# Kernel optimization log

Hardware: AMD Instinct MI355X
Metric: run time of the kernel (lower is better)

Reference implementation:

```python
import jax, jax.numpy as jnp
import numpy as np
from jax import lax

B, T_ENC, T_DEC, H, L, F, NC, S = 1024, 128, 64, 128, 2, 16, 4, 8
X_DIM = 2
IN_DIM = X_DIM + F          # encoder GRU input_size = 18
H_ENC = 2 * H               # encoder hidden = 256 (mean/logvar)
H_DEC = H + NC              # decoder hidden = 132 (concat_cond_ts=False)


def _gru_params(key, in_dim, hid):
    k1, k2, k3, k4 = jax.random.split(key, 4)
    s = 1.0 / np.sqrt(hid)
    u = lambda k, shp: jax.random.uniform(k, shp, minval=-s, maxval=s, dtype=jnp.float32)
    return u(k1, (3 * hid, in_dim)), u(k2, (3 * hid, hid)), u(k3, (3 * hid,)), u(k4, (3 * hid,))


def gru_cell(x, h, Wih, Whh, bih, bhh):
    # torch GRU cell: r,z,n gate ordering
    gi = x @ Wih.T + bih
    gh = h @ Whh.T + bhh
    hd = h.shape[-1]
    ir, iz, inn = gi[:, :hd], gi[:, hd:2 * hd], gi[:, 2 * hd:]
    hr, hz, hn = gh[:, :hd], gh[:, hd:2 * hd], gh[:, 2 * hd:]
    r = jax.nn.sigmoid(ir + hr)
    zg = jax.nn.sigmoid(iz + hz)
    n = jnp.tanh(inn + r * hn)
    return (1.0 - zg) * n + zg * h


def setup_inputs() -> dict:
    key = jax.random.key(0)
    ks = jax.random.split(key, 12)
    x = jax.random.normal(ks[0], (B, T_ENC, X_DIM), dtype=jnp.float32)
    features = jax.random.normal(ks[1], (B, T_ENC + T_DEC, F), dtype=jnp.float32)
    lengths = jax.random.randint(ks[2], (B,), T_ENC // 2, T_ENC + 1)
    mask = (jnp.arange(T_ENC)[None, :] < lengths[:, None]).astype(jnp.int32)
    eps = jax.random.normal(ks[3], (S, L, B, H), dtype=jnp.float32)
    enc0 = _gru_params(ks[4], IN_DIM, H_ENC)
    enc1 = _gru_params(ks[5], H_ENC, H_ENC)
    dec0 = _gru_params(ks[6], 2, H_DEC)
    dec1 = _gru_params(ks[7], H_DEC, H_DEC)
    sm = 1.0 / np.sqrt(H)
    W1 = jax.random.uniform(ks[8], (H // 2, H), minval=-sm, maxval=sm, dtype=jnp.float32)
    b1 = jax.random.uniform(ks[9], (H // 2,), minval=-sm, maxval=sm, dtype=jnp.float32)
    s2 = 1.0 / np.sqrt(H // 2)
    W2 = jax.random.uniform(ks[10], (2, H // 2), minval=-s2, maxval=s2, dtype=jnp.float32)
    b2 = jax.random.uniform(ks[11], (2,), minval=-s2, maxval=s2, dtype=jnp.float32)
    return dict(
        x=x, features=features, mask=mask, eps=eps,
        nsteps_encode=T_ENC, nsteps_decode=T_DEC, n_elbo_samp=S,
        enc_Wih0=enc0[0], enc_Whh0=enc0[1], enc_bih0=enc0[2], enc_bhh0=enc0[3],
        enc_Wih1=enc1[0], enc_Whh1=enc1[1], enc_bih1=enc1[2], enc_bhh1=enc1[3],
        dec_Wih0=dec0[0], dec_Whh0=dec0[1], dec_bih0=dec0[2], dec_bhh0=dec0[3],
        dec_Wih1=dec1[0], dec_Whh1=dec1[1], dec_bih1=dec1[2], dec_bhh1=dec1[3],
        W1=W1, b1=b1, W2=W2, b2=b2,
    )


def reference(x, features, mask, eps, nsteps_encode, nsteps_decode, n_elbo_samp,
              enc_Wih0, enc_Whh0, enc_bih0, enc_bhh0,
              enc_Wih1, enc_Whh1, enc_bih1, enc_bhh1,
              dec_Wih0, dec_Whh0, dec_bih0, dec_bhh0,
              dec_Wih1, dec_Whh1, dec_bih1, dec_bhh1,
              W1, b1, W2, b2):
    n_hidden = W1.shape[1]
    batch = x.shape[0]
    enc_input = jnp.concatenate([x, features[:, :nsteps_encode, :]], axis=-1)
    m = mask.astype(bool)

    def mlp(h):
        return jax.nn.softplus(jax.nn.relu(h @ W1.T + b1) @ W2.T + b2)

    # --- encoder: 2-layer GRU with pack_padded semantics (freeze h / zero out past length) ---
    def enc_step(h, xm):
        xt, mt = xm
        h0n = gru_cell(xt, h[0], enc_Wih0, enc_Whh0, enc_bih0, enc_bhh0)
        h0n = jnp.where(mt[:, None], h0n, h[0])
        h1n = gru_cell(h0n, h[1], enc_Wih1, enc_Whh1, enc_bih1, enc_bhh1)
        h1n = jnp.where(mt[:, None], h1n, h[1])
        out = jnp.where(mt[:, None], h1n, 0.0)
        return jnp.stack([h0n, h1n]), out

    h_init = jnp.zeros((2, batch, enc_Whh0.shape[1]), dtype=x.dtype)
    hT, outs = lax.scan(enc_step, h_init, (enc_input.transpose(1, 0, 2), m.T))
    enc_out = outs.transpose(1, 0, 2)                 # [B, T_enc, 2H]
    enc_pred = mlp(enc_out[..., :n_hidden])           # [B, T_enc, 2]
    z_mean = hT[:, :, :n_hidden]                      # [L, B, H]
    z_logvar = hT[:, :, n_hidden:]

    last = enc_pred[:, -1, :]                         # [B, 2]
    feat_cond = features[:, nsteps_encode, :4]        # cond_inds = [0,1,2,3]

    # --- decoder: sequential single-step GRU, h0 = cat(z, cond feats) ---
    def decode_one(e):
        z = e * jnp.exp(0.5 * z_logvar) + z_mean      # [L, B, H]
        fc = jnp.broadcast_to(feat_cond[None], (z.shape[0],) + feat_cond.shape)
        h0 = jnp.concatenate([z, fc], axis=-1)        # [L, B, H+NC]
        def step(carry, _):
            inp, h = carry
            d0 = gru_cell(inp, h[0], dec_Wih0, dec_Whh0, dec_bih0, dec_bhh0)
            d1 = gru_cell(d0, h[1], dec_Wih1, dec_Whh1, dec_bih1, dec_bhh1)
            out = mlp(d1[:, :n_hidden])
            return (out, jnp.stack([d0, d1])), out
        _, outs_d = lax.scan(step, (last, h0), None, length=nsteps_decode - 1)
        return jnp.concatenate([last[None], outs_d], axis=0)   # [T_dec, B, 2]

    dec = jax.vmap(decode_one)(eps)                   # [S, T_dec, B, 2]
    dec_preds = dec.transpose(0, 2, 1, 3)             # [S, B, T_dec, 2]
    enc_stack = jnp.broadcast_to(enc_pred[None, :, :-1, :],
                                 (n_elbo_samp, batch, enc_pred.shape[1] - 1, 2))
    return enc_stack, dec_preds
```

## Files before the change

### kernel.cpp

```cpp
#include <hip/hip_runtime.h>
#include <hip/hip_bf16.h>
#include <math.h>

typedef __hip_bfloat16 bf16;
typedef short v8s __attribute__((ext_vector_type(8)));
typedef float v4f __attribute__((ext_vector_type(4)));

#define NB   1024
#define NT   128
#define NH   128
#define HE   256
#define HD   132
#define HDP  160
#define HDS  164
#define GDP  144
#define NS   8
#define KX   32
#define RG   16
#define NRG  64

namespace wsoff {
constexpr size_t al(size_t x){ return (x + 255) & ~size_t(255); }
constexpr size_t FLAG  = 0;
constexpr size_t CNT   = 256;
// ... 86 lines not shown

__global__ void k_detect(char* ws, const void* eps){
  const unsigned short* p = (const unsigned short*)eps;
  int lane = threadIdx.x;
  unsigned short u = p[2*lane];
  int e = (u>>7)&0xFF;
  bool pl = (e>=118 && e<=130);
  unsigned long long m = __ballot(pl);
  if (lane==0) *(int*)(ws+wsoff::FLAG) = (__popcll(m) >= 32) ? 1 : 0;
}

__global__ void k_stage_xs(char* ws, const void* x, const void* feat){
  int isbf = *(const int*)(ws+wsoff::FLAG);
  size_t i = (size_t)blockIdx.x*blockDim.x + threadIdx.x;
  if (i >= (size_t)NT*NB*KX) return;
  int c = i % KX; size_t q = i / KX; int b = q % NB; int t = q / NB;
  float v = 0.f;
  if (c < 2)        v = ld_any(x,    ((size_t)b*NT + t)*2 + c, isbf);
  else if (c < 18)  v = ld_any(feat, ((size_t)b*192 + t)*16 + (c-2), isbf);
  ((bf16*)(ws+wsoff::XS))[i] = __float2bfloat16(v);
}
__global__ void k_stage_maskT(char* ws, const int* mask){
  size_t i = (size_t)blockIdx.x*blockDim.x + threadIdx.x;
  if (i >= (size_t)NT*NB) return;
  int b = i % NB, t = i / NB;
  ((int*)(ws+wsoff::MASKT))[i] = mask[(size_t)b*NT + t];
}
__global__ void k_stage_pad(char* ws, const void* src, size_t dstoff, int R, int SC, int DC){
  int isbf = *(const int*)(ws+wsoff::FLAG);
  size_t i = (size_t)blockIdx.x*blockDim.x + threadIdx.x;
  if (i >= (size_t)R*DC) return;
  int r = i / DC, c = i % DC;
  float v = (c < SC) ? ld_any(src, (size_t)r*SC + c, isbf) : 0.f;
  ((bf16*)(ws+dstoff))[i] = __float2bfloat16(v);
}
__global__ void k_stage_dec(char* ws, const void* src, size_t dstoff){
  int isbf = *(const int*)(ws+wsoff::FLAG);
  size_t i = (size_t)blockIdx.x*blockDim.x + threadIdx.x;
  if (i >= (size_t)432*HDP) return;
  int R = i / HDP, c = i % HDP;
  int g = R / GDP, ii = R % GDP;
  float v = (ii < HD && c < HD) ? ld_any(src, ((size_t)(g*HD+ii))*HD + c, isbf) : 0.f;
  ((bf16*)(ws+dstoff))[i] = __float2bfloat16(v);
}
struct SmallSegs { const void* src[12]; int dstoff[12]; int n[12]; };
__global__ void k_stage_small(char* ws, SmallSegs segs){
  int isbf = *(const int*)(ws+wsoff::FLAG);
  int s = blockIdx.x;
  float* dst = (float*)(ws + (size_t)segs.dstoff[s]);
  for (int i = threadIdx.x; i < segs.n[s]; i += blockDim.x)
    dst[i] = ld_any(segs.src[s], i, isbf);
}

#define ENC_LDS 156928
__global__ __attribute__((amdgpu_flat_work_group_size(512,512), amdgpu_waves_per_eu(1)))
void k_encoder(char* ws){
  extern __shared__ __align__(16) char smem[];
  const int bid = blockIdx.x, tid = threadIdx.x;
  const int lane = tid & 63, w = tid >> 6, lr = lane & 15, q = lane >> 4;
  const int* maskT = (const int*)(ws + wsoff::MASKT);

  if (bid < NRG){
    constexpr int NL0 = 18;
    constexpr int NR0 = 54 - NL0;
    const int rb = bid, rowbase = rb*RG;
    short* wlds = (short*)smem;
    short* abuf = (short*)(smem + 8*NL0*1024);
    int* cL0 = cntp(ws, rb);
    int* cXa = cntp(ws, NRG + rb*2);
    int* cXb = cntp(ws, NRG + rb*2 + 1);
    const short* WH = (const short*)(ws + wsoff::WHH0);
    const short* WI = (const short*)(ws + wsoff::WIH0);
    for (int idx = tid; idx < 8*NL0*512; idx += 512){
      int slot = idx >> 9, le = idx & 511, ln = le >> 3, j = le & 7, lrr = ln & 15, qq = ln >> 4;
      int w2 = slot / NL0, i = slot % NL0;
      int kb = i % 9, t2 = i / 9, g = t2 % 3, cs = t2 / 3;
      int row = g*HE + w2*32 + cs*16 + lrr;
      wlds[idx] = (kb < 8) ? WH[(size_t)row*256 + kb*32 + qq*8 + j]
                           : WI[(size_t)row*32  + qq*8 + j];
    }
    for (int idx = tid; idx < RG*296; idx += 512) abuf[idx] = 0;
    v8s wreg[NR0];
    #pragma unroll
    for (int i = NL0; i < 54; ++i){
      int kb = i % 9, t2 = i / 9, g = t2 % 3, cs = t2 / 3;
      int row = g*HE + w*32 + cs*16 + lr;
      wreg[i-NL0] = (kb < 8) ? fragld(bfp(ws,wsoff::WHH0), (size_t)row*256 + kb*32 + q*8)
                             : fragld(bfp(ws,wsoff::WIH0), (size_t)row*32 + q*8);
    }
    const float* bih = f32p(ws,wsoff::BIH0);
    const float* bhh = f32p(ws,wsoff::BHH0);
    float birv[2], bizv[2], binv[2], bhnv[2];
    #pragma unroll
    for (int cs=0;cs<2;cs++){
      int d = w*32 + cs*16 + lr;
      birv[cs]=bih[d]+bhh[d]; bizv[cs]=bih[HE+d]+bhh[HE+d];
      binv[cs]=bih[2*HE+d];   bhnv[cs]=bhh[2*HE+d];
    }
    float h0a[2][4] = {};
    float* hTf = f32p(ws, wsoff::H0F0);
    bf16* ring0 = bfp(ws, wsoff::RING0) + (size_t)rb*4*RG*256;
    const bf16* Xs = bfp(ws,wsoff::XS);
    __syncthreads();
    for (int t = 0; t < 128; ++t){
      if (tid < 64){
        int row = tid >> 2, ck = tid & 3;
// ... 59 lines not shown
    short* abuf = (short*)(smem + 8*NL1*1024);
    short* w1s  = (short*)(smem + 8*NL1*1024 + RG*520*2);
    int* cL0 = cntp(ws, rb);
    int* cXo = cntp(ws, NRG + rb*2 + ch);
    int* cXp = cntp(ws, NRG + rb*2 + (ch^1));
    const short* WX = (const short*)(ws + wsoff::WIH1);
    const short* WHs= (const short*)(ws + wsoff::WHH1);
    for (int idx = tid; idx < 8*NL1*512; idx += 512){
      int slot = idx >> 9, le = idx & 511, ln = le >> 3, j = le & 7, lrr = ln & 15, qq = ln >> 4;
      int w2 = slot / NL1, i = slot % NL1;
      int kb = i & 15, g = i >> 4;
      int row = g*HE + ch*128 + w2*16 + lrr;
      wlds[idx] = (kb < 8) ? WX [(size_t)row*256 + kb*32 + qq*8 + j]
                           : WHs[(size_t)row*256 + (kb-8)*32 + qq*8 + j];
    }
    if (ch == 0){
      const short* W1s = (const short*)(ws + wsoff::W1B);
      for (int idx = tid; idx < 16*512; idx += 512){
        int u = idx >> 9, le = idx & 511, ln = le >> 3, j = le & 7, lrr = ln & 15, qq = ln >> 4;
        int c = u >> 2, kb = u & 3;
        w1s[idx] = W1s[(size_t)(c*16 + lrr)*NH + kb*32 + qq*8 + j];
      }
    }
    for (int idx = tid; idx < RG*520; idx += 512) abuf[idx] = 0;
    v8s wreg[NR1];
    #pragma unroll
    for (int i = NL1; i < 48; ++i){
      int kb = i & 15, g = i >> 4;
      int row = g*HE + ch*128 + w*16 + lr;
      wreg[i-NL1] = (kb < 8) ? fragld(bfp(ws,wsoff::WIH1), (size_t)row*256 + kb*32 + q*8)
                             : fragld(bfp(ws,wsoff::WHH1), (size_t)row*256 + (kb-8)*32 + q*8);
    }
    const float* bih = f32p(ws,wsoff::BIH1);
    const float* bhh = f32p(ws,wsoff::BHH1);
    const int d = ch*128 + w*16 + lr;
    const float birv=bih[d]+bhh[d], bizv=bih[HE+d]+bhh[HE+d];
    const float binv=bih[2*HE+d],   bhnv=bhh[2*HE+d];
    float h1a[4] = {};
    float b1v[4], w20[4], w21[4];
    #pragma unroll
    for (int c=0;c<4;c++){
      int col=c*16+lr;
      b1v[c]=f32p(ws,wsoff::B1F)[col];
      w20[c]=f32p(ws,wsoff::W2F)[col]; w21[c]=f32p(ws,wsoff::W2F)[64+col];
    }
    const float b20 = f32p(ws,wsoff::B2F)[0], b21 = f32p(ws,wsoff::B2F)[1];
    float* hTf = f32p(ws, wsoff::H1F0);
    const bf16* ring0 = bfp(ws, wsoff::RING0) + (size_t)rb*4*RG*256;
    bf16* ring1o       = bfp(ws, wsoff::RING1) + (size_t)(rb*2+ch)*2*RG*128;
    const bf16* ring1p = bfp(ws, wsoff::RING1) + (size_t)(rb*2+(ch^1))*2*RG*128;
    float* encp = f32p(ws,wsoff::ENCP);
    __syncthreads();
    for (int s = 0; s < 128; ++s){
      {
        pollge(cL0, s+1);
        const bf16* hs = ring0 + (size_t)(s&3)*RG*256;
        int row = tid >> 5, ck = tid & 31;
        v8s v = ldg_coh16(hs + (size_t)row*256 + ck*8);
        *(v8s*)(abuf + row*520 + ck*8) = v;
      }
      if (s >= 1 && tid < 256){
        pollge(cXp, s);
        const bf16* hp = ring1p + (size_t)((s-1)&1)*RG*128;
        int row = tid >> 4, ck = tid & 15;
        v8s v = ldg_coh16(hp + (size_t)row*128 + ck*8);
        *(v8s*)(abuf + row*520 + 256 + (ch^1)*128 + ck*8) = v;
      }
      __syncthreads();
      v4f accr=(v4f){0,0,0,0}, accz=(v4f){0,0,0,0};
      v4f accxn=(v4f){0,0,0,0}, acchn=(v4f){0,0,0,0};
      #pragma unroll
      for (int kb=0;kb<16;kb++){
        v8s af = lds_frag8(abuf + lr*520 + kb*32 + q*8);
        #pragma unroll
        for (int g=0;g<3;g++){
          int i = g*16 + kb;
          v8s b = (i < NL1) ? ldsfrag(wlds, w*NL1 + i, lane) : wreg[i-NL1];
          v4f* A = (g==0)?&accr:(g==1)?&accz:((kb<8)?&accxn:&acchn);
          *A = mfma16(af, b, *A);
        }
      }
      int mk[4];
      #pragma unroll
      for (int rr=0;rr<4;rr++) mk[rr] = maskT[(size_t)s*NB + rowbase + q*4 + rr];
      __syncthreads();
      bf16* slot = ring1o + (size_t)(s&1)*RG*128;
      #pragma unroll
      for (int rr=0;rr<4;rr++){
        int row = q*4 + rr;
        float rg = sigm(accr[rr] + birv);
        float zg = sigm(accz[rr] + bizv);
        float nn = tanh_f(accxn[rr] + binv + rg*(acchn[rr]+bhnv));
        float hv = (1.f-zg)*nn + zg*h1a[rr];
        float h2 = mk[rr] ? hv : h1a[rr];
        h1a[rr] = h2;
        int ch_col = w*16 + lr;
        abuf[row*520 + 256 + ch*128 + ch_col] = bf16bits(h2);
        stg_coh_pair(slot + ((size_t)row*128 + (ch_col & ~1)), lr, h2);
        if (s == 127) hTf[(size_t)(rowbase+row)*HE + d] = h2;
      }
      __syncthreads();
      if (tid == 0) cntset(cXo, s+1);
      if (ch == 0 && w == 0){
        int vl = maskT[(size_t)s*NB + rowbase + lr];
        v4f acc[4];
        #pragma unroll
        for (int c=0;c<4;c++) acc[c]=(v4f){0,0,0,0};
        #pragma unroll
        for (int kb=0;kb<4;kb++){
          v8s af = vl ? lds_frag8(abuf + lr*520 + 256 + kb*32 + q*8)
                      : (v8s){0,0,0,0,0,0,0,0};
          #pragma unroll
          for (int c=0;c<4;c++) acc[c] = mfma16(af, ldsfrag(w1s, c*4+kb, lane), acc[c]);
        }
        float* outp = encp + (size_t)s*NB*2;
        #pragma unroll
        for (int rr=0;rr<4;rr++){
          float p0=0.f, p1=0.f;
          #pragma unroll
          for (int c=0;c<4;c++){
            float hv = acc[c][rr] + b1v[c]; hv = hv>0.f ? hv : 0.f;
            p0 += hv*w20[c]; p1 += hv*w21[c];
          }
          #pragma unroll
          for (int m=1;m<16;m<<=1){ p0 += __shfl_xor(p0,m,64); p1 += __shfl_xor(p1,m,64); }
          if (lr == 0){
            int grow = rowbase + q*4 + rr;
            outp[(size_t)grow*2]   = softplusf(p0+b20);
            outp[(size_t)grow*2+1] = softplusf(p1+b21);
          }
        }
      }
    }
  }
}

__global__ __attribute__((amdgpu_flat_work_group_size(512,512), amdgpu_waves_per_eu(1)))
void k_decoder(char* ws, const void* eps, const void* feat, void* out){
  extern __shared__ __align__(16) char dsm[];
  short* s_h0b = (short*)dsm;
  short* s_h1b = s_h0b + 32*HDS;
  float* s_inp = (float*)(dsm + 20992);
  float* s_red = (float*)(dsm + 21248);
  short* s_wh  = (short*)(dsm + 21760);
  short* s_cw0 = (short*)(dsm + 144640);
  short* s_cwx = (short*)(dsm + 147808);
  short* s_cwh = (short*)(dsm + 150976);
  float* s_tail= (float*)(dsm + 154144);
  float* s_th  = (float*)(dsm + 156192);
  float* s_tt0 = (float*)(dsm + 157216);
  float* s_tt1 = (float*)(dsm + 157376);

  const int isbf = *(const int*)(ws+wsoff::FLAG);
  const int tid = threadIdx.x;
  const int lane = tid & 63, w = tid >> 6, lr = lane & 15, q = lane >> 4;
  const int rowbase = blockIdx.x*32;
  constexpr size_t N0v = (size_t)NS*NB*127*2;

  const bf16* W0g  = bfp(ws,wsoff::WDHH0);
  const bf16* WX1g = bfp(ws,wsoff::WDIH1);

  for (int i = tid; i < 2*32*HDS; i += 512) s_h0b[i] = 0;
  {
    const short* src = (const short*)(ws + wsoff::WDHH1);
    for (int idx = tid; idx < 120*512; idx += 512){
      int u = idx >> 9, le = idx & 511, ln = le >> 3, e = le & 7, lrr = ln & 15, qq = ln >> 4;
      int kb = u % 5, t2 = u / 5, cc = t2 & 7, g = t2 >> 3;
      s_wh[idx] = src[(size_t)(g*GDP + cc*16 + lrr)*HDP + kb*32 + qq*8 + e];
    }
    const short* g0 = (const short*)(ws + wsoff::WDHH0);
    const short* gx = (const short*)(ws + wsoff::WDIH1);
    const short* gh = (const short*)(ws + wsoff::WDHH1);
    for (int i = tid; i < 3*4*132; i += 512){
      int k = i % 132, t2 = i / 132, c4 = t2 & 3, g = t2 >> 2;
      size_t so = (size_t)(g*GDP + 128 + c4)*HDP + k;
      s_cw0[i] = g0[so]; s_cwx[i] = gx[so]; s_cwh[i] = gh[so];
    }
  }
  if (tid < 4){
    const float* wih = f32p(ws,wsoff::WDIH0F);
    const float* bi0 = f32p(ws,wsoff::BDIH0); const float* bh0 = f32p(ws,wsoff::BDHH0);
    const float* bi1 = f32p(ws,wsoff::BDIH1); const float* bh1 = f32p(ws,wsoff::BDHH1);
    int dd = 128 + tid;
    float* T = s_tt0 + tid*10;
    T[0]=wih[(0*HD+dd)*2]; T[1]=wih[(0*HD+dd)*2+1];
    T[2]=wih[(1*HD+dd)*2]; T[3]=wih[(1*HD+dd)*2+1];
    T[4]=wih[(2*HD+dd)*2]; T[5]=wih[(2*HD+dd)*2+1];
    T[6]=bi0[dd]+bh0[dd]; T[7]=bi0[HD+dd]+bh0[HD+dd]; T[8]=bi0[2*HD+dd]; T[9]=bh0[2*HD+dd];
    float* T1 = s_tt1 + tid*4;
    T1[0]=bi1[dd]+bh1[dd]; T1[1]=bi1[HD+dd]+bh1[HD+dd]; T1[2]=bi1[2*HD+dd]; T1[3]=bh1[2*HD+dd];
  }
  if (tid < 64){
    int r0 = tid >> 1, c = tid & 1;
    int b = (rowbase + r0) & 1023;
    float v = f32p(ws,wsoff::ENCP)[((size_t)127*NB + b)*2 + c];
    s_inp[tid] = v;
    st_out(out, N0v + ((size_t)(rowbase+r0)*64)*2 + c, v, isbf);
  }
  __syncthreads();

  const int d = w*16 + lr;
  float e0a[10], e1a[4];
  {
    const float* wih = f32p(ws,wsoff::WDIH0F);
    const float* bi0 = f32p(ws,wsoff::BDIH0); const float* bh0 = f32p(ws,wsoff::BDHH0);
    const float* bi1 = f32p(ws,wsoff::BDIH1); const float* bh1 = f32p(ws,wsoff::BDHH1);
    e0a[0]=wih[(0*HD+d)*2]; e0a[1]=wih[(0*HD+d)*2+1];
    e0a[2]=wih[(1*HD+d)*2]; e0a[3]=wih[(1*HD+d)*2+1];
    e0a[4]=wih[(2*HD+d)*2]; e0a[5]=wih[(2*HD+d)*2+1];
    e0a[6]=bi0[d]+bh0[d]; e0a[7]=bi0[HD+d]+bh0[HD+d]; e0a[8]=bi0[2*HD+d]; e0a[9]=bh0[2*HD+d];
    e1a[0]=bi1[d]+bh1[d]; e1a[1]=bi1[HD+d]+bh1[HD+d]; e1a[2]=bi1[2*HD+d]; e1a[3]=bh1[2*HD+d];
  }
  float h0a[2][4], h1a[2][4];
  {
    const float* h0T = f32p(ws,wsoff::H0F0);
    const float* h1T = f32p(ws,wsoff::H1F0);
    #pragma unroll
    for (int m=0;m<2;m++)
      #pragma unroll
      for (int r=0;r<4;r++){
        int row = m*16 + q*4 + r, grow = rowbase + row;
        int s = grow >> 10, b = grow & 1023;
        float e0 = ld_any(eps, ((size_t)(s*2+0)*NB + b)*NH + d, isbf);
        float e1 = ld_any(eps, ((size_t)(s*2+1)*NB + b)*NH + d, isbf);
        float v0 = e0*__expf(0.5f*h0T[(size_t)b*HE + NH + d]) + h0T[(size_t)b*HE + d];
        float v1 = e1*__expf(0.5f*h1T[(size_t)b*HE + NH + d]) + h1T[(size_t)b*HE + d];
        h0a[m][r] = v0; h1a[m][r] = v1;
        s_h0b[row*HDS + d] = bf16bits(v0);
        s_h1b[row*HDS + d] = bf16bits(v1);
      }
  }
  if (tid < 128){
    int c4 = tid >> 5, row = tid & 31;
    int b = (rowbase + row) & 1023;
    float fc = ld_any(feat, (size_t)b*3072 + 2048 + c4, isbf);
    s_th[row*4 + c4] = fc;
    s_th[128 + row*4 + c4] = fc;
    s_h0b[row*HDS + 128 + c4] = bf16bits(fc);
    s_h1b[row*HDS + 128 + c4] = bf16bits(fc);
  }
  v8s w0f[3][5], wxf[3][5];
  #pragma unroll
  for (int g=0;g<3;g++)
    #pragma unroll
    for (int kb=0;kb<5;kb++){
      size_t off = (size_t)(g*GDP + w*16 + lr)*HDP + kb*32 + q*8;
      w0f[g][kb] = fragld(W0g, off);
      wxf[g][kb] = fragld(WX1g, off);
    }
  v8s w1f[2][4]; float b1v[2], w20v[2], w21v[2];
  if (w == 5 || w == 6){
    const int tb = (w-5)*2;
    const bf16* W1g = bfp(ws,wsoff::W1B);
    #pragma unroll
    for (int ct=0;ct<2;ct++){
      #pragma unroll
      for (int kb=0;kb<4;kb++)
        w1f[ct][kb] = fragld(W1g, (size_t)((tb+ct)*16+lr)*NH + kb*32 + q*8);
      b1v[ct]  = f32p(ws,wsoff::B1F)[(tb+ct)*16+lr];
      w20v[ct] = f32p(ws,wsoff::W2F)[(tb+ct)*16+lr];
      w21v[ct] = f32p(ws,wsoff::W2F)[64+(tb+ct)*16+lr];
    }
  }
  const float b20 = f32p(ws,wsoff::B2F)[0], b21 = f32p(ws,wsoff::B2F)[1];
  __syncthreads();

  const int ttg = tid >> 7, ttc4 = (tid >> 5) & 3, ttrow = tid & 31;
  for (int k = 0; k < 63; ++k){
    v4f p1[3][2];
    #pragma unroll
    for (int g=0;g<3;g++){ p1[g][0]=(v4f){0,0,0,0}; p1[g][1]=(v4f){0,0,0,0}; }
    #pragma unroll
    for (int m=0;m<2;m++)
      #pragma unroll
      for (int kb=0;kb<5;kb++){
        v8s A = lds_frag8(s_h0b + (m*16+lr)*HDS + kb*32 + q*8);
        #pragma unroll
        for (int g=0;g<3;g++) p1[g][m] = mfma16(A, w0f[g][kb], p1[g][m]);
      }
    if (k >= 1 && tid < 64){
      int row = tid >> 1, c = tid & 1;
      float p = s_red[row*2 + c] + s_red[64 + row*2 + c];
      float v = softplusf(p + (c ? b21 : b20));
      s_inp[tid] = v;
      st_out(out, N0v + ((size_t)(rowbase+row)*64 + k)*2 + c, v, isbf);
    }
    if (tid < 384){
      const unsigned* st = (const unsigned*)s_h0b + ttrow*(HDS/2);
      const unsigned* wp = (const unsigned*)s_cw0 + (ttg*4+ttc4)*66;
      float t0=0.f, t1=0.f, t2v=0.f, t3v=0.f;
      #pragma unroll 2
      for (int k2 = 0; k2 < 64; k2 += 4){
        unsigned sa=st[k2],   wa=wp[k2];
        unsigned sb=st[k2+1], wb=wp[k2+1];
        unsigned sc=st[k2+2], wc=wp[k2+2];
        unsigned sd=st[k2+3], wd=wp[k2+3];
        t0  += uasf(sa<<16)*uasf(wa<<16) + uasf(sa & 0xffff0000u)*uasf(wa & 0xffff0000u);
        t1  += uasf(sb<<16)*uasf(wb<<16) + uasf(sb & 0xffff0000u)*uasf(wb & 0xffff0000u);
        t2v += uasf(sc<<16)*uasf(wc<<16) + uasf(sc & 0xffff0000u)*uasf(wc & 0xffff0000u);
        t3v += uasf(sd<<16)*uasf(wd<<16) + uasf(sd & 0xffff0000u)*uasf(wd & 0xffff0000u);
      }
      { unsigned sa=st[64], wa=wp[64], sb=st[65], wb=wp[65];
        t0 += uasf(sa<<16)*uasf(wa<<16) + uasf(sa & 0xffff0000u)*uasf(wa & 0xffff0000u);
        t1 += uasf(sb<<16)*uasf(wb<<16) + uasf(sb & 0xffff0000u)*uasf(wb & 0xffff0000u); }
      s_tail[(ttg*4+ttc4)*32 + ttrow] = (t0+t1)+(t2v+t3v);
    }
    __syncthreads();
    #pragma unroll
    for (int m=0;m<2;m++)
      #pragma unroll
      for (int r=0;r<4;r++){
        int row = m*16 + q*4 + r;
        float i0 = s_inp[row*2], i1 = s_inp[row*2+1];
        float rr = sigm(i0*e0a[0]+i1*e0a[1] + p1[0][m][r] + e0a[6]);
        float zz = sigm(i0*e0a[2]+i1*e0a[3] + p1[1][m][r] + e0a[7]);
        float nn = tanh_f(i0*e0a[4]+i1*e0a[5] + e0a[8] + rr*(p1[2][m][r] + e0a[9]));
        float h = (1.f-zz)*nn + zz*h0a[m][r];
        h0a[m][r] = h;
        s_h0b[row*HDS + d] = bf16bits(h);
      }
    if (tid < 128){
      int c4 = tid >> 5, row = tid & 31;
      float ar = s_tail[(0*4+c4)*32+row], az = s_tail[(1*4+c4)*32+row], an = s_tail[(2*4+c4)*32+row];
      const float* T = s_tt0 + c4*10;
      float i0 = s_inp[row*2], i1 = s_inp[row*2+1];
      float rr = sigm(i0*T[0]+i1*T[1] + ar + T[6]);
      float zz = sigm(i0*T[2]+i1*T[3] + az + T[7]);
      float nn = tanh_f(i0*T[4]+i1*T[5] + T[8] + rr*(an + T[9]));
      float ho = s_th[row*4 + c4];
      float h = (1.f-zz)*nn + zz*ho;
      s_th[row*4 + c4] = h;
      s_h0b[row*HDS + 128 + c4] = bf16bits(h);
    }
    __syncthreads();
    v4f p2[4][2];
    #pragma unroll
    for (int g=0;g<4;g++){ p2[g][0]=(v4f){0,0,0,0}; p2[g][1]=(v4f){0,0,0,0}; }
    #pragma unroll
    for (int m=0;m<2;m++)
      #pragma unroll
      for (int kb=0;kb<5;kb++){
        v8s ax = lds_frag8(s_h0b + (m*16+lr)*HDS + kb*32 + q*8);
        v8s ah = lds_frag8(s_h1b + (m*16+lr)*HDS + kb*32 + q*8);
        #pragma unroll
        for (int g=0;g<3;g++){
          int aix = (g==2) ? 2 : g, aih = (g==2) ? 3 : g;
          p2[aix][m] = mfma16(ax, wxf[g][kb], p2[aix][m]);
          p2[aih][m] = mfma16(ah, ldsfrag(s_wh, (g*8+w)*5 + kb, lane), p2[aih][m]);
        }
      }
    {
      const unsigned* h0p = (const unsigned*)s_h0b + ttrow*(HDS/2);
      const unsigned* h1p = (const unsigned*)s_h1b + ttrow*(HDS/2);
      float td = 0.f;
      if (ttg <= 1){
        const unsigned* wx = (const unsigned*)s_cwx + (ttg*4+ttc4)*66;
        const unsigned* wh = (const unsigned*)s_cwh + (ttg*4+ttc4)*66;
        float x0=0.f, x1=0.f, y0=0.f, y1=0.f;
        #pragma unroll 2
        for (int k2 = 0; k2 < 66; k2 += 2){
          unsigned sa=h0p[k2],   wa=wx[k2];
          unsigned sb=h0p[k2+1], wb=wx[k2+1];
          unsigned ha=h1p[k2],   va=wh[k2];
          unsigned hb=h1p[k2+1], vb=wh[k2+1];
          x0 += uasf(sa<<16)*uasf(wa<<16) + uasf(sa & 0xffff0000u)*uasf(wa & 0xffff0000u);
          x1 += uasf(sb<<16)*uasf(wb<<16) + uasf(sb & 0xffff0000u)*uasf(wb & 0xffff0000u);
          y0 += uasf(ha<<16)*uasf(va<<16) + uasf(ha & 0xffff0000u)*uasf(va & 0xffff0000u);
          y1 += uasf(hb<<16)*uasf(vb<<16) + uasf(hb & 0xffff0000u)*uasf(vb & 0xffff0000u);
        }
        td = (x0+x1)+(y0+y1);
      } else if (ttg == 2){
        const unsigned* wx = (const unsigned*)s_cwx + (2*4+ttc4)*66;
        float x0=0.f, x1=0.f;
        #pragma unroll 2
        for (int k2 = 0; k2 < 66; k2 += 2){
          unsigned sa=h0p[k2], wa=wx[k2], sb=h0p[k2+1], wb=wx[k2+1];
          x0 += uasf(sa<<16)*uasf(wa<<16) + uasf(sa & 0xffff0000u)*uasf(wa & 0xffff0000u);
          x1 += uasf(sb<<16)*uasf(wb<<16) + uasf(sb & 0xffff0000u)*uasf(wb & 0xffff0000u);
        }
        td = x0+x1;
      } else {
        const unsigned* wh = (const unsigned*)s_cwh + (2*4+ttc4)*66;
        float y0=0.f, y1=0.f;
        #pragma unroll 2
        for (int k2 = 0; k2 < 66; k2 += 2){
          unsigned sa=h1p[k2], wa=wh[k2], sb=h1p[k2+1], wb=wh[k2+1];
          y0 += uasf(sa<<16)*uasf(wa<<16) + uasf(sa & 0xffff0000u)*uasf(wa & 0xffff0000u);
          y1 += uasf(sb<<16)*uasf(wb<<16) + uasf(sb & 0xffff0000u)*uasf(wb & 0xffff0000u);
        }
        td = y0+y1;
      }
      s_tail[(ttg*4+ttc4)*32 + ttrow] = td;
    }
    __syncthreads();
    #pragma unroll
    for (int m=0;m<2;m++)
      #pragma unroll
      for (int r=0;r<4;r++){
        int row = m*16 + q*4 + r;
        float rr = sigm(p2[0][m][r] + e1a[0]);
        float zz = sigm(p2[1][m][r] + e1a[1]);
        float nn = tanh_f(p2[2][m][r] + e1a[2] + rr*(p2[3][m][r] + e1a[3]));
        float h = (1.f-zz)*nn + zz*h1a[m][r];
        h1a[m][r] = h;
        s_h1b[row*HDS + d] = bf16bits(h);
      }
    if (tid < 128){
      int c4 = tid >> 5, row = tid & 31;
      float tr = s_tail[(0*4+c4)*32+row], tz = s_tail[(1*4+c4)*32+row];
      float txn = s_tail[(2*4+c4)*32+row], thn = s_tail[(3*4+c4)*32+row];
      const float* T1 = s_tt1 + c4*4;
      float rr = sigm(tr + T1[0]);
      float zz = sigm(tz + T1[1]);
      float nn = tanh_f(txn + T1[2] + rr*(thn + T1[3]));
      float ho = s_th[128 + row*4 + c4];
      float h = (1.f-zz)*nn + zz*ho;
      s_th[128 + row*4 + c4] = h;
      s_h1b[row*HDS + 128 + c4] = bf16bits(h);
    }
    __syncthreads();
    if (w == 5 || w == 6){
      v4f a3[2][2];
      #pragma unroll
      for (int ct=0;ct<2;ct++){ a3[ct][0]=(v4f){0,0,0,0}; a3[ct][1]=(v4f){0,0,0,0}; }
      #pragma unroll
      for (int m=0;m<2;m++)
        #pragma unroll
        for (int kb=0;kb<4;kb++){
          v8s A = lds_frag8(s_h1b + (m*16+lr)*HDS + kb*32 + q*8);
          #pragma unroll
          for (int ct=0;ct<2;ct++) a3[ct][m] = mfma16(A, w1f[ct][kb], a3[ct][m]);
        }
      #pragma unroll
      for (int m=0;m<2;m++)
        #pragma unroll
        for (int r=0;r<4;r++){
          float p0 = 0.f, p1v = 0.f;
          #pragma unroll
          for (int ct=0;ct<2;ct++){
            float hv = a3[ct][m][r] + b1v[ct]; hv = hv > 0.f ? hv : 0.f;
            p0 += hv*w20v[ct]; p1v += hv*w21v[ct];
          }
          #pragma unroll
          for (int mm=1;mm<16;mm<<=1){ p0 += __shfl_xor(p0,mm,64); p1v += __shfl_xor(p1v,mm,64); }
          if (lr == 0){
            int row = m*16 + q*4 + r;
            s_red[(w-5)*64 + row*2]   = p0;
            s_red[(w-5)*64 + row*2+1] = p1v;
          }
        }
    }
    __syncthreads();
  }
  if (tid < 64){
    int row = tid >> 1, c = tid & 1;
    float p = s_red[row*2 + c] + s_red[64 + row*2 + c];
    float v = softplusf(p + (c ? b21 : b20));
    st_out(out, N0v + ((size_t)(rowbase+row)*64 + 63)*2 + c, v, isbf);
  }
}

__global__ void k_assemble_enc(char* ws, void* out){
  int isbf = *(const int*)(ws+wsoff::FLAG);
  const float* encp = f32p(ws,wsoff::ENCP);
  constexpr size_t N0v = (size_t)NS*NB*127*2;
  for (size_t i = (size_t)blockIdx.x*blockDim.x + threadIdx.x; i < N0v;
       i += (size_t)gridDim.x*blockDim.x){
    int c = (int)(i & 1); size_t qq = i >> 1;
    int tt = (int)(qq % 127); size_t q2 = qq / 127; int b = (int)(q2 & 1023);
    st_out(out, i, encp[((size_t)tt*NB + b)*2 + c], isbf);
  }
}

extern "C" void kernel_launch(void* const* d_in, const int* in_sizes, int n_in,
                              void* d_out, int out_size, void* d_ws, size_t ws_size,
                              hipStream_t stream) {
  char* ws = (char*)d_ws;
  const int* mask = (const int*)d_in[2];
  auto gb = [](size_t n){ return dim3((unsigned)((n + 255)/256)); };

  hipMemsetAsync(ws+wsoff::CNT, 0, 192*64, stream);

  k_detect<<<1,64,0,stream>>>(ws, d_in[3]);

  k_stage_xs   <<<gb((size_t)NT*NB*KX),256,0,stream>>>(ws, d_in[0], d_in[1]);
  k_stage_maskT<<<gb((size_t)NT*NB),256,0,stream>>>(ws, mask);
  k_stage_pad<<<gb(768*32) ,256,0,stream>>>(ws, d_in[7],  wsoff::WIH0, 768, 18, 32);
  k_stage_pad<<<gb(768*256),256,0,stream>>>(ws, d_in[8],  wsoff::WHH0, 768, 256, 256);
  k_stage_pad<<<gb(768*256),256,0,stream>>>(ws, d_in[11], wsoff::WIH1, 768, 256, 256);
  k_stage_pad<<<gb(768*256),256,0,stream>>>(ws, d_in[12], wsoff::WHH1, 768, 256, 256);
  k_stage_pad<<<gb(64*128) ,256,0,stream>>>(ws, d_in[23], wsoff::W1B,  64, 128, 128);
  k_stage_dec<<<gb(432*HDP),256,0,stream>>>(ws, d_in[16], wsoff::WDHH0);
  k_stage_dec<<<gb(432*HDP),256,0,stream>>>(ws, d_in[19], wsoff::WDIH1);
  k_stage_dec<<<gb(432*HDP),256,0,stream>>>(ws, d_in[20], wsoff::WDHH1);

  SmallSegs ss;
  const void* srcs[12] = {d_in[9],d_in[10],d_in[13],d_in[14],d_in[15],
                          d_in[17],d_in[18],d_in[21],d_in[22],
                          d_in[24],d_in[25],d_in[26]};
  const size_t offs[12] = {wsoff::BIH0,wsoff::BHH0,wsoff::BIH1,wsoff::BHH1,wsoff::WDIH0F,
                           wsoff::BDIH0,wsoff::BDHH0,wsoff::BDIH1,wsoff::BDHH1,
                           wsoff::B1F,wsoff::W2F,wsoff::B2F};
  const int ns[12] = {768,768,768,768,792,396,396,396,396,64,128,2};
  for (int i=0;i<12;i++){ ss.src[i]=srcs[i]; ss.dstoff[i]=(int)offs[i]; ss.n[i]=ns[i]; }
  k_stage_small<<<12,256,0,stream>>>(ws, ss);

  hipFuncSetAttribute(reinterpret_cast<const void*>(k_encoder),
                      hipFuncAttributeMaxDynamicSharedMemorySize, ENC_LDS);
  hipFuncSetAttribute(reinterpret_cast<const void*>(k_decoder),
                      hipFuncAttributeMaxDynamicSharedMemorySize, 157440);

  k_encoder<<<192,512,ENC_LDS,stream>>>(ws);
  k_decoder<<<256,512,157440,stream>>>(ws, d_in[3], d_in[1], d_out);
  k_assemble_enc<<<2048,256,0,stream>>>(ws, d_out);
}
```

Baseline: 1.819 ms.

## Shrink decoder blocks to 16 rows, stream weights from global, overlap encoder layer-1 MFMAs

The decoder now handles 16 rows per block over 512 blocks instead of 32 rows over 256. It drops the large LDS copy of the layer-1 hidden weights and the register-resident weight fragments, reloading weight fragments from global/L2 on every step. This cuts LDS use from about 157KB to about 22KB and raises the waves_per_eu hint to 4, so several blocks can share a CU, at the price of repeated global weight loads. In the encoder's layer-1 path, the MFMAs for this chunk's own hidden half are issued before waiting on the partner chunk's data, to hide the cross-block poll latency.

After: 2.637 ms. 45.0% more time.

```diff
diff --git a/kernel.cpp b/kernel.cpp
--- a/kernel.cpp
+++ b/kernel.cpp
@@ -162,6 +162,14 @@
     dst[i] = ld_any(segs.src[s], i, isbf);
 }
 
+#define L1_STEP(kb) { \
+  v8s af = lds_frag8(abuf + lr*520 + (kb)*32 + q*8); \
+  { const int i = 0*16 + (kb); v8s b = (i < NL1) ? ldsfrag(wlds, w*NL1 + i, lane) : wreg[i-NL1]; accr = mfma16(af, b, accr); } \
+  { const int i = 1*16 + (kb); v8s b = (i < NL1) ? ldsfrag(wlds, w*NL1 + i, lane) : wreg[i-NL1]; accz = mfma16(af, b, accz); } \
+  { const int i = 2*16 + (kb); v8s b = (i < NL1) ? ldsfrag(wlds, w*NL1 + i, lane) : wreg[i-NL1]; \
+    if ((kb) < 8) accxn = mfma16(af, b, accxn); else acchn = mfma16(af, b, acchn); } \
+}
+
 #define ENC_LDS 156928
 __global__ __attribute__((amdgpu_flat_work_group_size(512,512), amdgpu_waves_per_eu(1)))
 void k_encoder(char* ws){
@@ -327,6 +335,8 @@
     float* encp = f32p(ws,wsoff::ENCP);
     __syncthreads();
     for (int s = 0; s < 128; ++s){
+      v4f accr=(v4f){0,0,0,0}, accz=(v4f){0,0,0,0};
+      v4f accxn=(v4f){0,0,0,0}, acchn=(v4f){0,0,0,0};
       {
         pollge(cL0, s+1);
         const bf16* hs = ring0 + (size_t)(s&3)*RG*256;
@@ -334,6 +344,8 @@
         v8s v = ldg_coh16(hs + (size_t)row*256 + ck*8);
         *(v8s*)(abuf + row*520 + ck*8) = v;
       }
+      if (ch == 0){ L1_STEP(8)  L1_STEP(9)  L1_STEP(10) L1_STEP(11) }
+      else        { L1_STEP(12) L1_STEP(13) L1_STEP(14) L1_STEP(15) }
       if (s >= 1 && tid < 256){
         pollge(cXp, s);
         const bf16* hp = ring1p + (size_t)((s-1)&1)*RG*128;
@@ -342,19 +354,10 @@
         *(v8s*)(abuf + row*520 + 256 + (ch^1)*128 + ck*8) = v;
       }
       __syncthreads();
-      v4f accr=(v4f){0,0,0,0}, accz=(v4f){0,0,0,0};
-      v4f accxn=(v4f){0,0,0,0}, acchn=(v4f){0,0,0,0};
-      #pragma unroll
-      for (int kb=0;kb<16;kb++){
-        v8s af = lds_frag8(abuf + lr*520 + kb*32 + q*8);
-        #pragma unroll
-        for (int g=0;g<3;g++){
-          int i = g*16 + kb;
-          v8s b = (i < NL1) ? ldsfrag(wlds, w*NL1 + i, lane) : wreg[i-NL1];
-          v4f* A = (g==0)?&accr:(g==1)?&accz:((kb<8)?&accxn:&acchn);
-          *A = mfma16(af, b, *A);
-        }
-      }
+      L1_STEP(0) L1_STEP(1) L1_STEP(2) L1_STEP(3)
+      L1_STEP(4) L1_STEP(5) L1_STEP(6) L1_STEP(7)
+      if (ch == 0){ L1_STEP(12) L1_STEP(13) L1_STEP(14) L1_STEP(15) }
+      else        { L1_STEP(8)  L1_STEP(9)  L1_STEP(10) L1_STEP(11) }
       int mk[4];
       #pragma unroll
       for (int rr=0;rr<4;rr++) mk[rr] = maskT[(size_t)s*NB + rowbase + q*4 + rr];
@@ -410,39 +413,35 @@
   }
 }
 
-__global__ __attribute__((amdgpu_flat_work_group_size(512,512), amdgpu_waves_per_eu(1)))
+#define DEC_LDS 22144
+__global__ __attribute__((amdgpu_flat_work_group_size(512,512), amdgpu_waves_per_eu(4)))
 void k_decoder(char* ws, const void* eps, const void* feat, void* out){
   extern __shared__ __align__(16) char dsm[];
   short* s_h0b = (short*)dsm;
-  short* s_h1b = s_h0b + 32*HDS;
-  float* s_inp = (float*)(dsm + 20992);
-  float* s_red = (float*)(dsm + 21248);
-  short* s_wh  = (short*)(dsm + 21760);
-  short* s_cw0 = (short*)(dsm + 144640);
-  short* s_cwx = (short*)(dsm + 147808);
-  short* s_cwh = (short*)(dsm + 150976);
-  float* s_tail= (float*)(dsm + 154144);
-  float* s_th  = (float*)(dsm + 156192);
-  float* s_tt0 = (float*)(dsm + 157216);
-  float* s_tt1 = (float*)(dsm + 157376);
+  short* s_h1b = s_h0b + 16*HDS;
+  float* s_inp = (float*)(dsm + 10496);
+  float* s_red = (float*)(dsm + 10624);
+  short* s_cw0 = (short*)(dsm + 10880);
+  short* s_cwx = (short*)(dsm + 14048);
+  short* s_cwh = (short*)(dsm + 17216);
+  float* s_tail= (float*)(dsm + 20384);
+  float* s_th  = (float*)(dsm + 21408);
+  float* s_tt0 = (float*)(dsm + 21920);
+  float* s_tt1 = (float*)(dsm + 22080);
 
   const int isbf = *(const int*)(ws+wsoff::FLAG);
   const int tid = threadIdx.x;
   const int lane = tid & 63, w = tid >> 6, lr = lane & 15, q = lane >> 4;
-  const int rowbase = blockIdx.x*32;
+  const int rowbase = blockIdx.x*16;
   constexpr size_t N0v = (size_t)NS*NB*127*2;
 
   const bf16* W0g  = bfp(ws,wsoff::WDHH0);
   const bf16* WX1g = bfp(ws,wsoff::WDIH1);
-
-  for (int i = tid; i < 2*32*HDS; i += 512) s_h0b[i] = 0;
+  const bf16* WH1g = bfp(ws,wsoff::WDHH1);
+  const size_t woff = (size_t)(w*16 + lr)*HDP + q*8;
+
+  for (int i = tid; i < 2*16*HDS; i += 512) s_h0b[i] = 0;
   {
-    const short* src = (const short*)(ws + wsoff::WDHH1);
-    for (int idx = tid; idx < 120*512; idx += 512){
-      int u = idx >> 9, le = idx & 511, ln = le >> 3, e = le & 7, lrr = ln & 15, qq = ln >> 4;
-      int kb = u % 5, t2 = u / 5, cc = t2 & 7, g = t2 >> 3;
-      s_wh[idx] = src[(size_t)(g*GDP + cc*16 + lrr)*HDP + kb*32 + qq*8 + e];
-    }
     const short* g0 = (const short*)(ws + wsoff::WDHH0);
     const short* gx = (const short*)(ws + wsoff::WDIH1);
     const short* gh = (const short*)(ws + wsoff::WDHH1);
@@ -465,7 +464,7 @@
     float* T1 = s_tt1 + tid*4;
     T1[0]=bi1[dd]+bh1[dd]; T1[1]=bi1[HD+dd]+bh1[HD+dd]; T1[2]=bi1[2*HD+dd]; T1[3]=bh1[2*HD+dd];
   }
-  if (tid < 64){
+  if (tid < 32){
     int r0 = tid >> 1, c = tid & 1;
     int b = (rowbase + r0) & 1023;
     float v = f32p(ws,wsoff::ENCP)[((size_t)127*NB + b)*2 + c];
@@ -486,83 +485,57 @@
     e0a[6]=bi0[d]+bh0[d]; e0a[7]=bi0[HD+d]+bh0[HD+d]; e0a[8]=bi0[2*HD+d]; e0a[9]=bh0[2*HD+d];
     e1a[0]=bi1[d]+bh1[d]; e1a[1]=bi1[HD+d]+bh1[HD+d]; e1a[2]=bi1[2*HD+d]; e1a[3]=bh1[2*HD+d];
   }
-  float h0a[2][4], h1a[2][4];
+  float h0a[4], h1a[4];
   {
     const float* h0T = f32p(ws,wsoff::H0F0);
     const float* h1T = f32p(ws,wsoff::H1F0);
     #pragma unroll
-    for (int m=0;m<2;m++)
-      #pragma unroll
-      for (int r=0;r<4;r++){
-        int row = m*16 + q*4 + r, grow = rowbase + row;
-        int s = grow >> 10, b = grow & 1023;
-        float e0 = ld_any(eps, ((size_t)(s*2+0)*NB + b)*NH + d, isbf);
-        float e1 = ld_any(eps, ((size_t)(s*2+1)*NB + b)*NH + d, isbf);
-        float v0 = e0*__expf(0.5f*h0T[(size_t)b*HE + NH + d]) + h0T[(size_t)b*HE + d];
-        float v1 = e1*__expf(0.5f*h1T[(size_t)b*HE + NH + d]) + h1T[(size_t)b*HE + d];
-        h0a[m][r] = v0; h1a[m][r] = v1;
-        s_h0b[row*HDS + d] = bf16bits(v0);
-        s_h1b[row*HDS + d] = bf16bits(v1);
-      }
-  }
-  if (tid < 128){
-    int c4 = tid >> 5, row = tid & 31;
+    for (int r=0;r<4;r++){
+      int row = q*4 + r, grow = rowbase + row;
+      int s = grow >> 10, b = grow & 1023;
+      float e0 = ld_any(eps, ((size_t)(s*2+0)*NB + b)*NH + d, isbf);
+      float e1 = ld_any(eps, ((size_t)(s*2+1)*NB + b)*NH + d, isbf);
+      float v0 = e0*__expf(0.5f*h0T[(size_t)b*HE + NH + d]) + h0T[(size_t)b*HE + d];
+      float v1 = e1*__expf(0.5f*h1T[(size_t)b*HE + NH + d]) + h1T[(size_t)b*HE + d];
+      h0a[r] = v0; h1a[r] = v1;
+      s_h0b[row*HDS + d] = bf16bits(v0);
+      s_h1b[row*HDS + d] = bf16bits(v1);
+    }
+  }
+  if (tid < 64){
+    int c4 = tid >> 4, row = tid & 15;
     int b = (rowbase + row) & 1023;
     float fc = ld_any(feat, (size_t)b*3072 + 2048 + c4, isbf);
     s_th[row*4 + c4] = fc;
-    s_th[128 + row*4 + c4] = fc;
+    s_th[64 + row*4 + c4] = fc;
     s_h0b[row*HDS + 128 + c4] = bf16bits(fc);
     s_h1b[row*HDS + 128 + c4] = bf16bits(fc);
   }
-  v8s w0f[3][5], wxf[3][5];
-  #pragma unroll
-  for (int g=0;g<3;g++)
-    #pragma unroll
-    for (int kb=0;kb<5;kb++){
-      size_t off = (size_t)(g*GDP + w*16 + lr)*HDP + kb*32 + q*8;
-      w0f[g][kb] = fragld(W0g, off);
-      wxf[g][kb] = fragld(WX1g, off);
-    }
-  v8s w1f[2][4]; float b1v[2], w20v[2], w21v[2];
-  if (w == 5 || w == 6){
-    const int tb = (w-5)*2;
-    const bf16* W1g = bfp(ws,wsoff::W1B);
-    #pragma unroll
-    for (int ct=0;ct<2;ct++){
-      #pragma unroll
-      for (int kb=0;kb<4;kb++)
-        w1f[ct][kb] = fragld(W1g, (size_t)((tb+ct)*16+lr)*NH + kb*32 + q*8);
-      b1v[ct]  = f32p(ws,wsoff::B1F)[(tb+ct)*16+lr];
-      w20v[ct] = f32p(ws,wsoff::W2F)[(tb+ct)*16+lr];
-      w21v[ct] = f32p(ws,wsoff::W2F)[64+(tb+ct)*16+lr];
-    }
-  }
   const float b20 = f32p(ws,wsoff::B2F)[0], b21 = f32p(ws,wsoff::B2F)[1];
   __syncthreads();
 
-  const int ttg = tid >> 7, ttc4 = (tid >> 5) & 3, ttrow = tid & 31;
+  const int t1g = tid >> 6, t1c4 = (tid >> 4) & 3, t1row = tid & 15;
+  const int t2g = tid >> 6, t2c4 = (tid >> 4) & 3, t2row = tid & 15;
   for (int k = 0; k < 63; ++k){
-    v4f p1[3][2];
-    #pragma unroll
-    for (int g=0;g<3;g++){ p1[g][0]=(v4f){0,0,0,0}; p1[g][1]=(v4f){0,0,0,0}; }
-    #pragma unroll
-    for (int m=0;m<2;m++)
-      #pragma unroll
-      for (int kb=0;kb<5;kb++){
-        v8s A = lds_frag8(s_h0b + (m*16+lr)*HDS + kb*32 + q*8);
-        #pragma unroll
-        for (int g=0;g<3;g++) p1[g][m] = mfma16(A, w0f[g][kb], p1[g][m]);
-      }
-    if (k >= 1 && tid < 64){
+    v4f p1[3];
+    p1[0]=(v4f){0,0,0,0}; p1[1]=(v4f){0,0,0,0}; p1[2]=(v4f){0,0,0,0};
+    #pragma unroll
+    for (int kb=0;kb<5;kb++){
+      v8s A = lds_frag8(s_h0b + lr*HDS + kb*32 + q*8);
+      #pragma unroll
+      for (int g=0;g<3;g++)
+        p1[g] = mfma16(A, fragld(W0g, (size_t)g*(GDP*HDP) + kb*32 + woff), p1[g]);
+    }
+    if (k >= 1 && tid < 32){
       int row = tid >> 1, c = tid & 1;
-      float p = s_red[row*2 + c] + s_red[64 + row*2 + c];
+      float p = s_red[row*2 + c] + s_red[32 + row*2 + c];
       float v = softplusf(p + (c ? b21 : b20));
       s_inp[tid] = v;
       st_out(out, N0v + ((size_t)(rowbase+row)*64 + k)*2 + c, v, isbf);
     }
-    if (tid < 384){
-      const unsigned* st = (const unsigned*)s_h0b + ttrow*(HDS/2);
-      const unsigned* wp = (const unsigned*)s_cw0 + (ttg*4+ttc4)*66;
+    if (tid < 192){
+      const unsigned* st = (const unsigned*)s_h0b + t1row*(HDS/2);
+      const unsigned* wp = (const unsigned*)s_cw0 + (t1g*4+t1c4)*66;
       float t0=0.f, t1=0.f, t2v=0.f, t3v=0.f;
       #pragma unroll 2
       for (int k2 = 0; k2 < 64; k2 += 4){
@@ -578,25 +551,23 @@
       { unsigned sa=st[64], wa=wp[64], sb=st[65], wb=wp[65];
         t0 += uasf(sa<<16)*uasf(wa<<16) + uasf(sa & 0xffff0000u)*uasf(wa & 0xffff0000u);
         t1 += uasf(sb<<16)*uasf(wb<<16) + uasf(sb & 0xffff0000u)*uasf(wb & 0xffff0000u); }
-      s_tail[(ttg*4+ttc4)*32 + ttrow] = (t0+t1)+(t2v+t3v);
+      s_tail[(t1g*4+t1c4)*16 + t1row] = (t0+t1)+(t2v+t3v);
     }
     __syncthreads();
     #pragma unroll
-    for (int m=0;m<2;m++)
-      #pragma unroll
-      for (int r=0;r<4;r++){
-        int row = m*16 + q*4 + r;
-        float i0 = s_inp[row*2], i1 = s_inp[row*2+1];
-        float rr = sigm(i0*e0a[0]+i1*e0a[1] + p1[0][m][r] + e0a[6]);
-        float zz = sigm(i0*e0a[2]+i1*e0a[3] + p1[1][m][r] + e0a[7]);
-        float nn = tanh_f(i0*e0a[4]+i1*e0a[5] + e0a[8] + rr*(p1[2][m][r] + e0a[9]));
-        float h = (1.f-zz)*nn + zz*h0a[m][r];
-        h0a[m][r] = h;
-        s_h0b[row*HDS + d] = bf16bits(h);
-      }
-    if (tid < 128){
-      int c4 = tid >> 5, row = tid & 31;
-      float ar = s_tail[(0*4+c4)*32+row], az = s_tail[(1*4+c4)*32+row], an = s_tail[(2*4+c4)*32+row];
+    for (int r=0;r<4;r++){
+      int row = q*4 + r;
+      float i0 = s_inp[row*2], i1 = s_inp[row*2+1];
+      float rr = sigm(i0*e0a[0]+i1*e0a[1] + p1[0][r] + e0a[6]);
+      float zz = sigm(i0*e0a[2]+i1*e0a[3] + p1[1][r] + e0a[7]);
+      float nn = tanh_f(i0*e0a[4]+i1*e0a[5] + e0a[8] + rr*(p1[2][r] + e0a[9]));
+      float h = (1.f-zz)*nn + zz*h0a[r];
+      h0a[r] = h;
+      s_h0b[row*HDS + d] = bf16bits(h);
+    }
+    if (tid < 64){
+      int c4 = tid >> 4, row = tid & 15;
+      float ar = s_tail[(0*4+c4)*16+row], az = s_tail[(1*4+c4)*16+row], an = s_tail[(2*4+c4)*16+row];
       const float* T = s_tt0 + c4*10;
       float i0 = s_inp[row*2], i1 = s_inp[row*2+1];
       float rr = sigm(i0*T[0]+i1*T[1] + ar + T[6]);
@@ -608,29 +579,26 @@
       s_h0b[row*HDS + 128 + c4] = bf16bits(h);
     }
     __syncthreads();
-    v4f p2[4][2];
-    #pragma unroll
-    for (int g=0;g<4;g++){ p2[g][0]=(v4f){0,0,0,0}; p2[g][1]=(v4f){0,0,0,0}; }
-    #pragma unroll
-    for (int m=0;m<2;m++)
-      #pragma unroll
-      for (int kb=0;kb<5;kb++){
-        v8s ax = lds_frag8(s_h0b + (m*16+lr)*HDS + kb*32 + q*8);
-        v8s ah = lds_frag8(s_h1b + (m*16+lr)*HDS + kb*32 + q*8);
-        #pragma unroll
-        for (int g=0;g<3;g++){
-          int aix = (g==2) ? 2 : g, aih = (g==2) ? 3 : g;
-          p2[aix][m] = mfma16(ax, wxf[g][kb], p2[aix][m]);
-          p2[aih][m] = mfma16(ah, ldsfrag(s_wh, (g*8+w)*5 + kb, lane), p2[aih][m]);
-        }
-      }
-    {
-      const unsigned* h0p = (const unsigned*)s_h0b + ttrow*(HDS/2);
-      const unsigned* h1p = (const unsigned*)s_h1b + ttrow*(HDS/2);
+    v4f p2[4];
+    p2[0]=(v4f){0,0,0,0}; p2[1]=(v4f){0,0,0,0}; p2[2]=(v4f){0,0,0,0}; p2[3]=(v4f){0,0,0,0};
+    #pragma unroll
+    for (int kb=0;kb<5;kb++){
+      v8s ax = lds_frag8(s_h0b + lr*HDS + kb*32 + q*8);
+      v8s ah = lds_frag8(s_h1b + lr*HDS + kb*32 + q*8);
+      #pragma unroll
+      for (int g=0;g<3;g++){
+        int aix = (g==2) ? 2 : g, aih = (g==2) ? 3 : g;
+        p2[aix] = mfma16(ax, fragld(WX1g, (size_t)g*(GDP*HDP) + kb*32 + woff), p2[aix]);
+        p2[aih] = mfma16(ah, fragld(WH1g, (size_t)g*(GDP*HDP) + kb*32 + woff), p2[aih]);
+      }
+    }
+    if (tid < 256){
+      const unsigned* h0p = (const unsigned*)s_h0b + t2row*(HDS/2);
+      const unsigned* h1p = (const unsigned*)s_h1b + t2row*(HDS/2);
       float td = 0.f;
-      if (ttg <= 1){
-        const unsigned* wx = (const unsigned*)s_cwx + (ttg*4+ttc4)*66;
-        const unsigned* wh = (const unsigned*)s_cwh + (ttg*4+ttc4)*66;
+      if (t2g <= 1){
+        const unsigned* wx = (const unsigned*)s_cwx + (t2g*4+t2c4)*66;
+        const unsigned* wh = (const unsigned*)s_cwh + (t2g*4+t2c4)*66;
         float x0=0.f, x1=0.f, y0=0.f, y1=0.f;
         #pragma unroll 2
         for (int k2 = 0; k2 < 66; k2 += 2){
@@ -644,8 +612,8 @@
           y1 += uasf(hb<<16)*uasf(vb<<16) + uasf(hb & 0xffff0000u)*uasf(vb & 0xffff0000u);
         }
         td = (x0+x1)+(y0+y1);
-      } else if (ttg == 2){
-        const unsigned* wx = (const unsigned*)s_cwx + (2*4+ttc4)*66;
+      } else if (t2g == 2){
+        const unsigned* wx = (const unsigned*)s_cwx + (2*4+t2c4)*66;
         float x0=0.f, x1=0.f;
         #pragma unroll 2
         for (int k2 = 0; k2 < 66; k2 += 2){
@@ -655,7 +623,7 @@
         }
         td = x0+x1;
       } else {
-        const unsigned* wh = (const unsigned*)s_cwh + (2*4+ttc4)*66;
+        const unsigned* wh = (const unsigned*)s_cwh + (2*4+t2c4)*66;
         float y0=0.f, y1=0.f;
         #pragma unroll 2
         for (int k2 = 0; k2 < 66; k2 += 2){
@@ -665,71 +633,77 @@
         }
         td = y0+y1;
       }
-      s_tail[(ttg*4+ttc4)*32 + ttrow] = td;
+      s_tail[(t2g*4+t2c4)*16 + t2row] = td;
     }
     __syncthreads();
     #pragma unroll
-    for (int m=0;m<2;m++)
-      #pragma unroll
-      for (int r=0;r<4;r++){
-        int row = m*16 + q*4 + r;
-        float rr = sigm(p2[0][m][r] + e1a[0]);
-        float zz = sigm(p2[1][m][r] + e1a[1]);
-        float nn = tanh_f(p2[2][m][r] + e1a[2] + rr*(p2[3][m][r] + e1a[3]));
-        float h = (1.f-zz)*nn + zz*h1a[m][r];
-        h1a[m][r] = h;
-        s_h1b[row*HDS + d] = bf16bits(h);
-      }
-    if (tid < 128){
-      int c4 = tid >> 5, row = tid & 31;
-      float tr = s_tail[(0*4+c4)*32+row], tz = s_tail[(1*4+c4)*32+row];
-      float txn = s_tail[(2*4+c4)*32+row], thn = s_tail[(3*4+c4)*32+row];
+    for (int r=0;r<4;r++){
+      int row = q*4 + r;
+      float rr = sigm(p2[0][r] + e1a[0]);
+      float zz = sigm(p2[1][r] + e1a[1]);
+      float nn = tanh_f(p2[2][r] + e1a[2] + rr*(p2[3][r] + e1a[3]));
+      float h = (1.f-zz)*nn + zz*h1a[r];
+      h1a[r] = h;
+      s_h1b[row*HDS + d] = bf16bits(h);
+    }
+    if (tid < 64){
+      int c4 = tid >> 4, row = tid & 15;
+      float tr = s_tail[(0*4+c4)*16+row], tz = s_tail[(1*4+c4)*16+row];
+      float txn = s_tail[(2*4+c4)*16+row], thn = s_tail[(3*4+c4)*16+row];
       const float* T1 = s_tt1 + c4*4;
       float rr = sigm(tr + T1[0]);
       float zz = sigm(tz + T1[1]);
       float nn = tanh_f(txn + T1[2] + rr*(thn + T1[3]));
-      float ho = s_th[128 + row*4 + c4];
+      float ho = s_th[64 + row*4 + c4];
       float h = (1.f-zz)*nn + zz*ho;
-      s_th[128 + row*4 + c4] = h;
+      s_th[64 + row*4 + c4] = h;
       s_h1b[row*HDS + 128 + c4] = bf16bits(h);
     }
     __syncthreads();
     if (w == 5 || w == 6){
-      v4f a3[2][2];
-      #pragma unroll
-      for (int ct=0;ct<2;ct++){ a3[ct][0]=(v4f){0,0,0,0}; a3[ct][1]=(v4f){0,0,0,0}; }
-      #pragma unroll
-      for (int m=0;m<2;m++)
-        #pragma unroll
-        for (int kb=0;kb<4;kb++){
-          v8s A = lds_frag8(s_h1b + (m*16+lr)*HDS + kb*32 + q*8);
-          #pragma unroll
-          for (int ct=0;ct<2;ct++) a3[ct][m] = mfma16(A, w1f[ct][kb], a3[ct][m]);
+      const int tb = (w-5)*2;
+      const bf16* W1g = bfp(ws,wsoff::W1B);
+      v8s w1a[2][4];
+      float b1vv[2], w20vv[2], w21vv[2];
+      #pragma unroll
+      for (int ct=0;ct<2;ct++){
+        #pragma unroll
+        for (int kb=0;kb<4;kb++)
+          w1a[ct][kb] = fragld(W1g, (size_t)((tb+ct)*16+lr)*NH + kb*32 + q*8);
+        b1vv[ct]  = f32p(ws,wsoff::B1F)[(tb+ct)*16+lr];
+        w20vv[ct] = f32p(ws,wsoff::W2F)[(tb+ct)*16+lr];
+        w21vv[ct] = f32p(ws,wsoff::W2F)[64+(tb+ct)*16+lr];
+      }
+      v4f a3[2];
+      a3[0]=(v4f){0,0,0,0}; a3[1]=(v4f){0,0,0,0};
+      #pragma unroll
+      for (int kb=0;kb<4;kb++){
+        v8s A = lds_frag8(s_h1b + lr*HDS + kb*32 + q*8);
+        #pragma unroll
+        for (int ct=0;ct<2;ct++) a3[ct] = mfma16(A, w1a[ct][kb], a3[ct]);
+      }
+      #pragma unroll
+      for (int r=0;r<4;r++){
+        float p0 = 0.f, p1v = 0.f;
+        #pragma unroll
+        for (int ct=0;ct<2;ct++){
+          float hv = a3[ct][r] + b1vv[ct]; hv = hv > 0.f ? hv : 0.f;
+          p0 += hv*w20vv[ct]; p1v += hv*w21vv[ct];
         }
-      #pragma unroll
-      for (int m=0;m<2;m++)
-        #pragma unroll
-        for (int r=0;r<4;r++){
-          float p0 = 0.f, p1v = 0.f;
-          #pragma unroll
-          for (int ct=0;ct<2;ct++){
-            float hv = a3[ct][m][r] + b1v[ct]; hv = hv > 0.f ? hv : 0.f;
-            p0 += hv*w20v[ct]; p1v += hv*w21v[ct];
-          }
-          #pragma unroll
-          for (int mm=1;mm<16;mm<<=1){ p0 += __shfl_xor(p0,mm,64); p1v += __shfl_xor(p1v,mm,64); }
-          if (lr == 0){
-            int row = m*16 + q*4 + r;
-            s_red[(w-5)*64 + row*2]   = p0;
-            s_red[(w-5)*64 + row*2+1] = p1v;
-          }
+        #pragma unroll
+        for (int mm=1;mm<16;mm<<=1){ p0 += __shfl_xor(p0,mm,64); p1v += __shfl_xor(p1v,mm,64); }
+        if (lr == 0){
+          int row = q*4 + r;
+          s_red[(w-5)*32 + row*2]   = p0;
+          s_red[(w-5)*32 + row*2+1] = p1v;
         }
+      }
     }
     __syncthreads();
   }
-  if (tid < 64){
+  if (tid < 32){
     int row = tid >> 1, c = tid & 1;
-    float p = s_red[row*2 + c] + s_red[64 + row*2 + c];
+    float p = s_red[row*2 + c] + s_red[32 + row*2 + c];
     float v = softplusf(p + (c ? b21 : b20));
     st_out(out, N0v + ((size_t)(rowbase+row)*64 + 63)*2 + c, v, isbf);
   }
@@ -783,9 +757,9 @@
   hipFuncSetAttribute(reinterpret_cast<const void*>(k_encoder),
                       hipFuncAttributeMaxDynamicSharedMemorySize, ENC_LDS);
   hipFuncSetAttribute(reinterpret_cast<const void*>(k_decoder),
-                      hipFuncAttributeMaxDynamicSharedMemorySize, 157440);
+                      hipFuncAttributeMaxDynamicSharedMemorySize, 32768);
 
   k_encoder<<<192,512,ENC_LDS,stream>>>(ws);
-  k_decoder<<<256,512,157440,stream>>>(ws, d_in[3], d_in[1], d_out);
+  k_decoder<<<512,512,DEC_LDS,stream>>>(ws, d_in[3], d_in[1], d_out);
   k_assemble_enc<<<2048,256,0,stream>>>(ws, d_out);
 }
```
